# Kernel optimization log

Hardware: AMD Instinct MI355X
Metric: run time of the kernel (lower is better)

## Reference

```python
import jax, jax.numpy as jnp
import numpy as np

N_NODES = 100000


def gcn_conv(x, W, b, src, dst, n):
    # PyG GCNConv: h = x @ W; add self-loops; sym-normalize; scatter-add to dst; + bias
    h = x @ W  # [N, out]
    loops = jnp.arange(n, dtype=src.dtype)
    src2 = jnp.concatenate([src, loops])
    dst2 = jnp.concatenate([dst, loops])
    deg = jax.ops.segment_sum(jnp.ones_like(dst2, dtype=h.dtype), dst2, num_segments=n)
    dinv = jnp.where(deg > 0, jax.lax.rsqrt(deg), 0.0)
    norm = dinv[src2] * dinv[dst2]  # [E+N]
    msg = h[src2] * norm[:, None]   # gather + scale
    out = jax.ops.segment_sum(msg, dst2, num_segments=n)  # scatter-add
    return out + b


def setup_inputs() -> dict:
    key = jax.random.key(0)
    k = jax.random.split(key, 6)
    N, F_IN, H, E = N_NODES, 128, 100, 3200000
    x = jax.random.normal(k[0], (N, F_IN), dtype=jnp.float32)
    edge_index = jax.random.randint(k[1], (2, E), 0, N, dtype=jnp.int64)
    W1 = jax.random.normal(k[2], (F_IN, H), dtype=jnp.float32) / np.sqrt(F_IN).astype(np.float32)
    b1 = jax.random.normal(k[3], (H,), dtype=jnp.float32) * 0.01
    W2 = jax.random.normal(k[4], (H, 1), dtype=jnp.float32) / np.sqrt(H).astype(np.float32)
    b2 = jax.random.normal(k[5], (1,), dtype=jnp.float32) * 0.01
    return {"x": x, "edge_index": edge_index, "W1": W1, "b1": b1, "W2": W2, "b2": b2}


def reference(x, edge_index, W1, b1, W2, b2) -> jnp.ndarray:
    src, dst = edge_index[0], edge_index[1]
    h = gcn_conv(x, W1, b1, src, dst, N_NODES)
    h = jax.nn.relu(h)
    out = gcn_conv(h, W2, b2, src, dst, N_NODES)  # [N, 1]
    return out
```

## Files before the change

kernel.cpp:

```cpp
#include <hip/hip_runtime.h>

#define F_IN 128
#define H1 100
#define G1LD 128
#define CAP 80
#define CH_A 4096
#define NBIN_MAX 256

__device__ __forceinline__ unsigned short f2bf(float f) {
    union { float f; unsigned u; } x;
    x.f = f;
    unsigned u = x.u;
    u += 0x7FFF + ((u >> 16) & 1);
    return (unsigned short)(u >> 16);
}
__device__ __forceinline__ float bflo(unsigned v) {
    union { unsigned u; float f; } x;
    x.u = v << 16;
    return x.f;
}
__device__ __forceinline__ float bfhi(unsigned v) {
    union { unsigned u; float f; } x;
    x.u = v & 0xFFFF0000u;
    return x.f;
}

__global__ __launch_bounds__(256) void k_histA(const int* __restrict__ dst, int* __restrict__ M,
                                               int E, int n, int nbin, int nbA) {
    __shared__ int hist[NBIN_MAX];
    const int tid = threadIdx.x;
    hist[tid] = 0;
    __syncthreads();
    const int base = blockIdx.x * CH_A;
    const int lim = min(CH_A, E - base);
    for (int j = tid; j < lim; j += 256) {
        unsigned d = (unsigned)dst[base + j];
        if (d >= (unsigned)n) d = 0;
        atomicAdd(&hist[d >> 9], 1);
    }
    __syncthreads();
    for (int b = tid; b < nbin; b += 256) M[b * nbA + blockIdx.x] = hist[b];
}

__global__ __launch_bounds__(256) void k_scanRows(const int* __restrict__ M,
                                                  int* __restrict__ Mscan,
                                                  int* __restrict__ T, int nbA) {
    __shared__ int sd[256];
    const int tid = threadIdx.x;
    const int b = blockIdx.x;
    const int base = tid * 4;
    int c[4];
    int s = 0;
    #pragma unroll
    for (int j = 0; j < 4; ++j) {
        int i = base + j;
        c[j] = (i < nbA) ? M[b * nbA + i] : 0;
        s += c[j];
    }
    const int own = s;
    sd[tid] = s;
    __syncthreads();
    for (int off = 1; off < 256; off <<= 1) {
        int t = (tid >= off) ? sd[tid - off] : 0;
        __syncthreads();
        sd[tid] += t;
        __syncthreads();
    }
    int pre = sd[tid] - own;
    #pragma unroll
    for (int j = 0; j < 4; ++j) {
        int i = base + j;
        if (i < nbA) {
            Mscan[b * nbA + i] = pre;
            pre += c[j];
        }
    }
    if (tid == 255) T[b] = sd[255];
}

__global__ __launch_bounds__(256) void k_scanBins(const int* __restrict__ T,
                                                  int* __restrict__ binBase, int nbin) {
    __shared__ int sd[256];
    const int tid = threadIdx.x;
    const int v = (tid < nbin) ? T[tid] : 0;
    sd[tid] = v;
    __syncthreads();
    for (int off = 1; off < 256; off <<= 1) {
        int t = (tid >= off) ? sd[tid - off] : 0;
        __syncthreads();
        sd[tid] += t;
        __syncthreads();
    }
    if (tid < nbin) binBase[tid] = sd[tid] - v;
}

__global__ __launch_bounds__(256) void k_binC(const int* __restrict__ src, const int* __restrict__ dst,
                                              const int* __restrict__ Mscan, const int* __restrict__ binBase,
                                              unsigned* __restrict__ pk, int E, int n, int nbin, int nbA) {
    __shared__ int hist[NBIN_MAX];
    __shared__ int loff[NBIN_MAX];
    const int tid = threadIdx.x;
    hist[tid] = 0;
    for (int b = tid; b < nbin; b += 256) loff[b] = binBase[b] + Mscan[b * nbA + blockIdx.x];
    __syncthreads();
    const int base = blockIdx.x * CH_A;
    const int lim = min(CH_A, E - base);
    for (int j = tid; j < lim; j += 256) {
        unsigned d = (unsigned)dst[base + j];
        unsigned s = (unsigned)src[base + j];
        if (d >= (unsigned)n) d = 0;
        if (s >= (unsigned)n) s = 0;
        const int bin = d >> 9;
        const int r = atomicAdd(&hist[bin], 1);
        pk[loff[bin] + r] = (s << 9) | (d & 511u);
    }
}

__global__ __launch_bounds__(512) void k_binD(const unsigned* __restrict__ pk,
                                              const int* __restrict__ binBase,
                                              int* __restrict__ ebuf, int* __restrict__ counts,
                                              int E, int n, int nbin) {
    __shared__ int fcnt[512];
    const int tid = threadIdx.x;
    fcnt[tid] = 0;
    __syncthreads();
    const int b = blockIdx.x;
    const int bstart = binBase[b];
    const int bend = (b + 1 < nbin) ? binBase[b + 1] : E;
    for (int j = bstart + tid; j < bend; j += 512) {
        const unsigned v = pk[j];
        const int dlow = (int)(v & 511u);
        const int s = (int)(v >> 9);
        const int r = atomicAdd(&fcnt[dlow], 1);
        if (r < CAP) ebuf[((b << 9) + dlow) * CAP + r] = s;
    }
    __syncthreads();
    const int d = (b << 9) + tid;
    if (d < n) {
        const int c = min(fcnt[tid], CAP);
        counts[d] = fcnt[tid];
        const int cp = min((c + 15) & ~15, CAP);
        int* __restrict__ row = ebuf + d * CAP;
        for (int r = c; r < cp; ++r) row[r] = n;
    }
}

__global__ __launch_bounds__(128) void k_gemm1(
    const float* __restrict__ x, const float* __restrict__ W1,
    const int* __restrict__ counts, unsigned short* __restrict__ g, int n) {
    __shared__ float xs[16][F_IN];
    const int f = threadIdx.x;
    const int nb = blockIdx.x * 16;

    {
        const float4* xv = (const float4*)(x + (long)nb * F_IN);
        float4* xsv = (float4*)&xs[0][0];
        #pragma unroll
        for (int k = 0; k < 4; ++k) {
            const int i = f + k * 128;
            const int node = nb + (i >> 5);
            xsv[i] = (node < n) ? xv[i] : make_float4(0.f, 0.f, 0.f, 0.f);
        }
    }
    __syncthreads();

    const bool act = (f < H1);
    float accv[16];
    #pragma unroll
    for (int v = 0; v < 16; ++v) accv[v] = 0.f;

    for (int kc = 0; kc < F_IN; kc += 8) {
        float w[8];
        #pragma unroll
        for (int j = 0; j < 8; ++j) w[j] = act ? W1[(kc + j) * H1 + f] : 0.0f;
        #pragma unroll
        for (int v = 0; v < 16; ++v) {
            const float4 b0 = *(const float4*)&xs[v][kc];
            const float4 b1 = *(const float4*)&xs[v][kc + 4];
            float s = accv[v];
            s = fmaf(b0.x, w[0], s);
            s = fmaf(b0.y, w[1], s);
            s = fmaf(b0.z, w[2], s);
            s = fmaf(b0.w, w[3], s);
            s = fmaf(b1.x, w[4], s);
            s = fmaf(b1.y, w[5], s);
            s = fmaf(b1.z, w[6], s);
            s = fmaf(b1.w, w[7], s);
            accv[v] = s;
        }
    }

    if (act) {
        #pragma unroll
        for (int v = 0; v < 16; ++v) {
            const int node = nb + v;
            if (node < n) {
                const float di = rsqrtf(1.0f + (float)counts[node]);
                g[(node << 7) + f] = f2bf(accv[v] * di);
            } else if (node == n) {
                g[(node << 7) + f] = 0;
            }
        }
    }
}

__global__ __launch_bounds__(256) void k_agg1(
    const unsigned short* __restrict__ g1, const int* __restrict__ counts,
    const int* __restrict__ ebuf,
    const float* __restrict__ b1, const float* __restrict__ W2,
    float* __restrict__ g2, int n) {
    const int lane = threadIdx.x & 63;
    const int node = blockIdx.x * 4 + (threadIdx.x >> 6);
    if (node >= n) return;

    const int c = counts[node];
    const int cnt = (c < CAP) ? c : CAP;
    const int cntp = min((cnt + 15) & ~15, CAP);
    const int4* __restrict__ ebq = (const int4*)(ebuf + node * CAP);
    const unsigned* __restrict__ gp = (const unsigned*)g1;

    const unsigned v0 = gp[(node << 6) + lane];
    float pa0 = bflo(v0), pa1 = 0.f, pa2 = 0.f, pa3 = 0.f;
    float pb0 = bfhi(v0), pb1 = 0.f, pb2 = 0.f, pb3 = 0.f;

    for (int j = 0; j < cntp; j += 16) {
        const int4 e0 = ebq[(j >> 2)];
        const int4 e1 = ebq[(j >> 2) + 1];
        const int4 e2 = ebq[(j >> 2) + 2];
        const int4 e3 = ebq[(j >> 2) + 3];
        const unsigned w0 = gp[(e0.x << 6) + lane];
        const unsigned w1 = gp[(e0.y << 6) + lane];
        const unsigned w2 = gp[(e0.z << 6) + lane];
        const unsigned w3 = gp[(e0.w << 6) + lane];
        const unsigned w4 = gp[(e1.x << 6) + lane];
        const unsigned w5 = gp[(e1.y << 6) + lane];
        const unsigned w6 = gp[(e1.z << 6) + lane];
        const unsigned w7 = gp[(e1.w << 6) + lane];
        const unsigned w8 = gp[(e2.x << 6) + lane];
        const unsigned w9 = gp[(e2.y << 6) + lane];
        const unsigned wa = gp[(e2.z << 6) + lane];
        const unsigned wb = gp[(e2.w << 6) + lane];
        const unsigned wc = gp[(e3.x << 6) + lane];
        const unsigned wd = gp[(e3.y << 6) + lane];
        const unsigned we = gp[(e3.z << 6) + lane];
        const unsigned wf = gp[(e3.w << 6) + lane];
        pa0 += bflo(w0); pb0 += bfhi(w0);
        pa1 += bflo(w1); pb1 += bfhi(w1);
        pa2 += bflo(w2); pb2 += bfhi(w2);
        pa3 += bflo(w3); pb3 += bfhi(w3);
        pa0 += bflo(w4); pb0 += bfhi(w4);
        pa1 += bflo(w5); pb1 += bfhi(w5);
        pa2 += bflo(w6); pb2 += bfhi(w6);
        pa3 += bflo(w7); pb3 += bfhi(w7);
        pa0 += bflo(w8); pb0 += bfhi(w8);
        pa1 += bflo(w9); pb1 += bfhi(w9);
        pa2 += bflo(wa); pb2 += bfhi(wa);
        pa3 += bflo(wb); pb3 += bfhi(wb);
        pa0 += bflo(wc); pb0 += bfhi(wc);
        pa1 += bflo(wd); pb1 += bfhi(wd);
        pa2 += bflo(we); pb2 += bfhi(we);
        pa3 += bflo(wf); pb3 += bfhi(wf);
    }

    const float di = rsqrtf(1.0f + (float)c);
    float sum = 0.f;
    if (lane < H1 / 2) {
        const float sa = (pa0 + pa1) + (pa2 + pa3);
        const float sb = (pb0 + pb1) + (pb2 + pb3);
        const float2 bb = ((const float2*)b1)[lane];
        const float2 ww = ((const float2*)W2)[lane];
        sum = fmaxf(fmaf(di, sa, bb.x), 0.f) * ww.x + fmaxf(fmaf(di, sb, bb.y), 0.f) * ww.y;
    }
    #pragma unroll
    for (int off = 32; off > 0; off >>= 1) sum += __shfl_down(sum, off);
    if (lane == 0) g2[node] = di * sum;
}

__global__ __launch_bounds__(256) void k_agg2(
    const float* __restrict__ g2, const int* __restrict__ counts,
    const int* __restrict__ ebuf, const float* __restrict__ b2,
    float* __restrict__ out, int n) {
    const int lane = threadIdx.x & 63;
    const int node = blockIdx.x * 4 + (threadIdx.x >> 6);
    if (node >= n) return;
    const int c = counts[node];
    const int cnt = (c < CAP) ? c : CAP;
    const int* __restrict__ eb = ebuf + node * CAP;
    float s = 0.f;
    for (int j = lane; j < cnt; j += 64) s += g2[eb[j]];
    #pragma unroll
    for (int off = 32; off > 0; off >>= 1) s += __shfl_down(s, off);
    if (lane == 0) {
        float di = rsqrtf(1.0f + (float)c);
        out[node] = fmaf(di, g2[node] + s, b2[0]);
    }
}

extern "C" void kernel_launch(void* const* d_in, const int* in_sizes, int n_in,
                              void* d_out, int out_size, void* d_ws, size_t ws_size,
                              hipStream_t stream) {
    const float* x  = (const float*)d_in[0];
    const int*   ei = (const int*)d_in[1];
    const float* W1 = (const float*)d_in[2];
    const float* b1 = (const float*)d_in[3];
    const float* W2 = (const float*)d_in[4];
    const float* b2 = (const float*)d_in[5];

    const int n = in_sizes[0] / F_IN;
    const int E = in_sizes[1] / 2;
    const int* src = ei;
    const int* dst = ei + E;

    const int nbin = (n + 511) >> 9;
    const int nbA  = (E + CH_A - 1) / CH_A;
    const int m    = nbin * nbA;

    char* p = (char*)d_ws;
    int* counts = (int*)p;                   p += (size_t)n * 4;
    float* g2   = (float*)p;                 p += (size_t)n * 4;
    p = (char*)(((size_t)p + 255) & ~(size_t)255);
    unsigned short* g1 = (unsigned short*)p; p += (size_t)(n + 1) * G1LD * 2;
    p = (char*)(((size_t)p + 255) & ~(size_t)255);
    int* ebuf   = (int*)p;                   p += (size_t)n * CAP * 4;
    unsigned* pk = (unsigned*)p;             p += (size_t)E * 4;
    int* M      = (int*)p;                   p += (size_t)m * 4;
    int* Mscan  = (int*)p;                   p += (size_t)m * 4;
    int* T      = (int*)p;                   p += 1024;
    int* binBase = (int*)p;                  p += 1024;
    float* out = (float*)d_out;

    k_histA<<<nbA, 256, 0, stream>>>(dst, M, E, n, nbin, nbA);
    k_scanRows<<<nbin, 256, 0, stream>>>(M, Mscan, T, nbA);
    k_scanBins<<<1, 256, 0, stream>>>(T, binBase, nbin);
    k_binC<<<nbA, 256, 0, stream>>>(src, dst, Mscan, binBase, pk, E, n, nbin, nbA);
    k_binD<<<nbin, 512, 0, stream>>>(pk, binBase, ebuf, counts, E, n, nbin);
    k_gemm1<<<(n + 16) / 16, 128, 0, stream>>>(x, W1, counts, g1, n);
    k_agg1<<<(n + 3) / 4, 256, 0, stream>>>(g1, counts, ebuf, b1, W2, g2, n);
    k_agg2<<<(n + 3) / 4, 256, 0, stream>>>(g2, counts, ebuf, b2, out, n);
}
```

Before: 357.5 us.

## Register-tile GEMM1 4x4, pack 4 nodes per wave with 16B gathers in agg1

The first-layer GEMM now uses a 4-node by 4-feature register tile per thread over 20-node blocks, with float4 loads of W1 and vectorized bf16 stores. The first aggregation assigns 16 lanes per node, so each wave handles 4 nodes and each lane gathers a 16-byte uint4 of bf16 features per neighbor. Padding of edge lists in binD is dropped; out-of-range slots are instead masked to a dummy zero row inside agg1. The aim is fewer wasted lanes on 100-wide rows and better load efficiency, at the cost of loops that run to the largest neighbor count among the 4 nodes in a wave.

```diff
diff --git a/kernel.cpp b/kernel.cpp
--- a/kernel.cpp
+++ b/kernel.cpp
@@ -6,6 +6,7 @@
 #define CAP 80
 #define CH_A 4096
 #define NBIN_MAX 256
+#define GN 20
 
 __device__ __forceinline__ unsigned short f2bf(float f) {
     union { float f; unsigned u; } x;
@@ -136,69 +137,78 @@
     }
     __syncthreads();
     const int d = (b << 9) + tid;
-    if (d < n) {
-        const int c = min(fcnt[tid], CAP);
-        counts[d] = fcnt[tid];
-        const int cp = min((c + 15) & ~15, CAP);
-        int* __restrict__ row = ebuf + d * CAP;
-        for (int r = c; r < cp; ++r) row[r] = n;
-    }
+    if (d < n) counts[d] = fcnt[tid];
 }
 
 __global__ __launch_bounds__(128) void k_gemm1(
     const float* __restrict__ x, const float* __restrict__ W1,
     const int* __restrict__ counts, unsigned short* __restrict__ g, int n) {
-    __shared__ float xs[16][F_IN];
-    const int f = threadIdx.x;
-    const int nb = blockIdx.x * 16;
+    __shared__ float xs[GN][132];
+    const int t = threadIdx.x;
+    const int nb = blockIdx.x * GN;
 
     {
-        const float4* xv = (const float4*)(x + (long)nb * F_IN);
-        float4* xsv = (float4*)&xs[0][0];
+        const float4* xv = (const float4*)(x + (size_t)nb * F_IN);
+        for (int i = t; i < GN * 32; i += 128) {
+            const int v = i >> 5, kq = i & 31;
+            const int node = nb + v;
+            const float4 val = (node < n) ? xv[i] : make_float4(0.f, 0.f, 0.f, 0.f);
+            *(float4*)&xs[v][kq * 4] = val;
+        }
+    }
+    __syncthreads();
+
+    const bool act = (t < 125);
+    const int fi = t % 25;
+    const int vg = min(t / 25, 4);
+    const int f0 = fi * 4, v0 = vg * 4;
+
+    float acc[4][4];
+    #pragma unroll
+    for (int i = 0; i < 4; ++i)
         #pragma unroll
-        for (int k = 0; k < 4; ++k) {
-            const int i = f + k * 128;
-            const int node = nb + (i >> 5);
-            xsv[i] = (node < n) ? xv[i] : make_float4(0.f, 0.f, 0.f, 0.f);
-        }
-    }
-    __syncthreads();
-
-    const bool act = (f < H1);
-    float accv[16];
-    #pragma unroll
-    for (int v = 0; v < 16; ++v) accv[v] = 0.f;
-
-    for (int kc = 0; kc < F_IN; kc += 8) {
-        float w[8];
-        #pragma unroll
-        for (int j = 0; j < 8; ++j) w[j] = act ? W1[(kc + j) * H1 + f] : 0.0f;
-        #pragma unroll
-        for (int v = 0; v < 16; ++v) {
-            const float4 b0 = *(const float4*)&xs[v][kc];
-            const float4 b1 = *(const float4*)&xs[v][kc + 4];
-            float s = accv[v];
-            s = fmaf(b0.x, w[0], s);
-            s = fmaf(b0.y, w[1], s);
-            s = fmaf(b0.z, w[2], s);
-            s = fmaf(b0.w, w[3], s);
-            s = fmaf(b1.x, w[4], s);
-            s = fmaf(b1.y, w[5], s);
-            s = fmaf(b1.z, w[6], s);
-            s = fmaf(b1.w, w[7], s);
-            accv[v] = s;
-        }
+        for (int j = 0; j < 4; ++j) acc[i][j] = 0.f;
+
+    const float4* __restrict__ Wf4 = (const float4*)W1;
+    #pragma unroll 4
+    for (int k = 0; k < F_IN; ++k) {
+        const float4 wv = Wf4[k * 25 + fi];
+        const float x0 = xs[v0][k];
+        const float x1 = xs[v0 + 1][k];
+        const float x2 = xs[v0 + 2][k];
+        const float x3 = xs[v0 + 3][k];
+        acc[0][0] = fmaf(x0, wv.x, acc[0][0]);
+        acc[0][1] = fmaf(x0, wv.y, acc[0][1]);
+        acc[0][2] = fmaf(x0, wv.z, acc[0][2]);
+        acc[0][3] = fmaf(x0, wv.w, acc[0][3]);
+        acc[1][0] = fmaf(x1, wv.x, acc[1][0]);
+        acc[1][1] = fmaf(x1, wv.y, acc[1][1]);
+        acc[1][2] = fmaf(x1, wv.z, acc[1][2]);
+        acc[1][3] = fmaf(x1, wv.w, acc[1][3]);
+        acc[2][0] = fmaf(x2, wv.x, acc[2][0]);
+        acc[2][1] = fmaf(x2, wv.y, acc[2][1]);
+        acc[2][2] = fmaf(x2, wv.z, acc[2][2]);
+        acc[2][3] = fmaf(x2, wv.w, acc[2][3]);
+        acc[3][0] = fmaf(x3, wv.x, acc[3][0]);
+        acc[3][1] = fmaf(x3, wv.y, acc[3][1]);
+        acc[3][2] = fmaf(x3, wv.z, acc[3][2]);
+        acc[3][3] = fmaf(x3, wv.w, acc[3][3]);
     }
 
     if (act) {
         #pragma unroll
-        for (int v = 0; v < 16; ++v) {
-            const int node = nb + v;
+        for (int i = 0; i < 4; ++i) {
+            const int node = nb + v0 + i;
             if (node < n) {
                 const float di = rsqrtf(1.0f + (float)counts[node]);
-                g[(node << 7) + f] = f2bf(accv[v] * di);
+                ushort4 o;
+                o.x = f2bf(acc[i][0] * di);
+                o.y = f2bf(acc[i][1] * di);
+                o.z = f2bf(acc[i][2] * di);
+                o.w = f2bf(acc[i][3] * di);
+                *(ushort4*)&g[(node << 7) + f0] = o;
             } else if (node == n) {
-                g[(node << 7) + f] = 0;
+                *(ushort4*)&g[(node << 7) + f0] = make_ushort4(0, 0, 0, 0);
             }
         }
     }
@@ -210,70 +220,64 @@
     const float* __restrict__ b1, const float* __restrict__ W2,
     float* __restrict__ g2, int n) {
     const int lane = threadIdx.x & 63;
-    const int node = blockIdx.x * 4 + (threadIdx.x >> 6);
-    if (node >= n) return;
-
-    const int c = counts[node];
-    const int cnt = (c < CAP) ? c : CAP;
-    const int cntp = min((cnt + 15) & ~15, CAP);
-    const int4* __restrict__ ebq = (const int4*)(ebuf + node * CAP);
-    const unsigned* __restrict__ gp = (const unsigned*)g1;
-
-    const unsigned v0 = gp[(node << 6) + lane];
-    float pa0 = bflo(v0), pa1 = 0.f, pa2 = 0.f, pa3 = 0.f;
-    float pb0 = bfhi(v0), pb1 = 0.f, pb2 = 0.f, pb3 = 0.f;
-
-    for (int j = 0; j < cntp; j += 16) {
-        const int4 e0 = ebq[(j >> 2)];
-        const int4 e1 = ebq[(j >> 2) + 1];
-        const int4 e2 = ebq[(j >> 2) + 2];
-        const int4 e3 = ebq[(j >> 2) + 3];
-        const unsigned w0 = gp[(e0.x << 6) + lane];
-        const unsigned w1 = gp[(e0.y << 6) + lane];
-        const unsigned w2 = gp[(e0.z << 6) + lane];
-        const unsigned w3 = gp[(e0.w << 6) + lane];
-        const unsigned w4 = gp[(e1.x << 6) + lane];
-        const unsigned w5 = gp[(e1.y << 6) + lane];
-        const unsigned w6 = gp[(e1.z << 6) + lane];
-        const unsigned w7 = gp[(e1.w << 6) + lane];
-        const unsigned w8 = gp[(e2.x << 6) + lane];
-        const unsigned w9 = gp[(e2.y << 6) + lane];
-        const unsigned wa = gp[(e2.z << 6) + lane];
-        const unsigned wb = gp[(e2.w << 6) + lane];
-        const unsigned wc = gp[(e3.x << 6) + lane];
-        const unsigned wd = gp[(e3.y << 6) + lane];
-        const unsigned we = gp[(e3.z << 6) + lane];
-        const unsigned wf = gp[(e3.w << 6) + lane];
-        pa0 += bflo(w0); pb0 += bfhi(w0);
-        pa1 += bflo(w1); pb1 += bfhi(w1);
-        pa2 += bflo(w2); pb2 += bfhi(w2);
-        pa3 += bflo(w3); pb3 += bfhi(w3);
-        pa0 += bflo(w4); pb0 += bfhi(w4);
-        pa1 += bflo(w5); pb1 += bfhi(w5);
-        pa2 += bflo(w6); pb2 += bfhi(w6);
-        pa3 += bflo(w7); pb3 += bfhi(w7);
-        pa0 += bflo(w8); pb0 += bfhi(w8);
-        pa1 += bflo(w9); pb1 += bfhi(w9);
-        pa2 += bflo(wa); pb2 += bfhi(wa);
-        pa3 += bflo(wb); pb3 += bfhi(wb);
-        pa0 += bflo(wc); pb0 += bfhi(wc);
-        pa1 += bflo(wd); pb1 += bfhi(wd);
-        pa2 += bflo(we); pb2 += bfhi(we);
-        pa3 += bflo(wf); pb3 += bfhi(wf);
+    const int fl = lane & 15;
+    const int wave = threadIdx.x >> 6;
+    const int node = blockIdx.x * 16 + wave * 4 + (lane >> 4);
+    const int nodec = min(node, n - 1);
+
+    const int c = counts[nodec];
+    const int cnt = min(c, CAP);
+    int cmax = cnt;
+    cmax = max(cmax, __shfl_xor(cmax, 16));
+    cmax = max(cmax, __shfl_xor(cmax, 32));
+
+    const int* __restrict__ eb = ebuf + nodec * CAP;
+    const uint4* __restrict__ gp = (const uint4*)g1;
+
+    uint4 w = gp[(nodec << 4) + fl];
+    float2 a0 = make_float2(bflo(w.x), bfhi(w.x));
+    float2 a1 = make_float2(bflo(w.y), bfhi(w.y));
+    float2 a2 = make_float2(bflo(w.z), bfhi(w.z));
+    float2 a3 = make_float2(bflo(w.w), bfhi(w.w));
+
+    #pragma unroll 2
+    for (int j = 0; j < cmax; ++j) {
+        int e = eb[j];
+        e = (j < cnt) ? e : n;
+        w = gp[(e << 4) + fl];
+        a0.x += bflo(w.x); a0.y += bfhi(w.x);
+        a1.x += bflo(w.y); a1.y += bfhi(w.y);
+        a2.x += bflo(w.z); a2.y += bfhi(w.z);
+        a3.x += bflo(w.w); a3.y += bfhi(w.w);
     }
 
     const float di = rsqrtf(1.0f + (float)c);
     float sum = 0.f;
-    if (lane < H1 / 2) {
-        const float sa = (pa0 + pa1) + (pa2 + pa3);
-        const float sb = (pb0 + pb1) + (pb2 + pb3);
-        const float2 bb = ((const float2*)b1)[lane];
-        const float2 ww = ((const float2*)W2)[lane];
-        sum = fmaxf(fmaf(di, sa, bb.x), 0.f) * ww.x + fmaxf(fmaf(di, sb, bb.y), 0.f) * ww.y;
-    }
-    #pragma unroll
-    for (int off = 32; off > 0; off >>= 1) sum += __shfl_down(sum, off);
-    if (lane == 0) g2[node] = di * sum;
+    const int fbase = fl * 8;
+    if (fbase < H1) {
+        const float4 ba = ((const float4*)b1)[fl * 2];
+        const float4 wa = ((const float4*)W2)[fl * 2];
+        float s;
+        s  = fmaxf(fmaf(di, a0.x, ba.x), 0.f) * wa.x;
+        s += fmaxf(fmaf(di, a0.y, ba.y), 0.f) * wa.y;
+        s += fmaxf(fmaf(di, a1.x, ba.z), 0.f) * wa.z;
+        s += fmaxf(fmaf(di, a1.y, ba.w), 0.f) * wa.w;
+        sum = s;
+        if (fbase + 4 < H1) {
+            const float4 bb = ((const float4*)b1)[fl * 2 + 1];
+            const float4 wb = ((const float4*)W2)[fl * 2 + 1];
+            s  = fmaxf(fmaf(di, a2.x, bb.x), 0.f) * wb.x;
+            s += fmaxf(fmaf(di, a2.y, bb.y), 0.f) * wb.y;
+            s += fmaxf(fmaf(di, a3.x, bb.z), 0.f) * wb.z;
+            s += fmaxf(fmaf(di, a3.y, bb.w), 0.f) * wb.w;
+            sum += s;
+        }
+    }
+    sum += __shfl_xor(sum, 1);
+    sum += __shfl_xor(sum, 2);
+    sum += __shfl_xor(sum, 4);
+    sum += __shfl_xor(sum, 8);
+    if (fl == 0 && node < n) g2[node] = di * sum;
 }
 
 __global__ __launch_bounds__(256) void k_agg2(
@@ -334,7 +338,7 @@
     k_scanBins<<<1, 256, 0, stream>>>(T, binBase, nbin);
     k_binC<<<nbA, 256, 0, stream>>>(src, dst, Mscan, binBase, pk, E, n, nbin, nbA);
     k_binD<<<nbin, 512, 0, stream>>>(pk, binBase, ebuf, counts, E, n, nbin);
-    k_gemm1<<<(n + 16) / 16, 128, 0, stream>>>(x, W1, counts, g1, n);
-    k_agg1<<<(n + 3) / 4, 256, 0, stream>>>(g1, counts, ebuf, b1, W2, g2, n);
+    k_gemm1<<<(n + GN) / GN, 128, 0, stream>>>(x, W1, counts, g1, n);
+    k_agg1<<<(n + 15) / 16, 256, 0, stream>>>(g1, counts, ebuf, b1, W2, g2, n);
     k_agg2<<<(n + 3) / 4, 256, 0, stream>>>(g2, counts, ebuf, b2, out, n);
 }
```

Result: no change. 350.6 us (-1.9%).

## Stage binning scatter in LDS and retile GEMM1 to 4x4 register blocks

Applied to the files above, without the earlier changes.

The binning scatter kernel now uses larger chunks of 15360 edges per 512-thread block. It counting-sorts each chunk into shared memory first, then writes runs to global memory that are contiguous per bin, which makes the previously scattered global stores coalesced. The first GEMM is retiled so each thread computes a 4-node by 4-feature block using float4 loads of W1 and padded shared rows, with vectorized bf16 stores. This adds a serial prefix scan by a single thread, binary searches per element, large LDS usage that lowers occupancy, and a second read of dst.

```diff
diff --git a/kernel.cpp b/kernel.cpp
--- a/kernel.cpp
+++ b/kernel.cpp
@@ -4,8 +4,9 @@
 #define H1 100
 #define G1LD 128
 #define CAP 80
-#define CH_A 4096
+#define CH_S 15360
 #define NBIN_MAX 256
+#define GN 20
 
 __device__ __forceinline__ unsigned short f2bf(float f) {
     union { float f; unsigned u; } x;
@@ -25,21 +26,21 @@
     return x.f;
 }
 
-__global__ __launch_bounds__(256) void k_histA(const int* __restrict__ dst, int* __restrict__ M,
+__global__ __launch_bounds__(512) void k_histA(const int* __restrict__ dst, int* __restrict__ M,
                                                int E, int n, int nbin, int nbA) {
     __shared__ int hist[NBIN_MAX];
     const int tid = threadIdx.x;
-    hist[tid] = 0;
-    __syncthreads();
-    const int base = blockIdx.x * CH_A;
-    const int lim = min(CH_A, E - base);
-    for (int j = tid; j < lim; j += 256) {
+    for (int b = tid; b < nbin; b += 512) hist[b] = 0;
+    __syncthreads();
+    const int base = blockIdx.x * CH_S;
+    const int lim = min(CH_S, E - base);
+    for (int j = tid; j < lim; j += 512) {
         unsigned d = (unsigned)dst[base + j];
         if (d >= (unsigned)n) d = 0;
         atomicAdd(&hist[d >> 9], 1);
     }
     __syncthreads();
-    for (int b = tid; b < nbin; b += 256) M[b * nbA + blockIdx.x] = hist[b];
+    for (int b = tid; b < nbin; b += 512) M[b * nbA + blockIdx.x] = hist[b];
 }
 
 __global__ __launch_bounds__(256) void k_scanRows(const int* __restrict__ M,
@@ -94,25 +95,55 @@
     if (tid < nbin) binBase[tid] = sd[tid] - v;
 }
 
-__global__ __launch_bounds__(256) void k_binC(const int* __restrict__ src, const int* __restrict__ dst,
-                                              const int* __restrict__ Mscan, const int* __restrict__ binBase,
-                                              unsigned* __restrict__ pk, int E, int n, int nbin, int nbA) {
+__global__ __launch_bounds__(512) void k_sortC(const int* __restrict__ src, const int* __restrict__ dst,
+                                               const int* __restrict__ Mscan, const int* __restrict__ binBase,
+                                               unsigned* __restrict__ pk, int E, int n, int nbin, int nbA) {
+    __shared__ unsigned staged[CH_S];
     __shared__ int hist[NBIN_MAX];
+    __shared__ int offs[NBIN_MAX + 1];
     __shared__ int loff[NBIN_MAX];
     const int tid = threadIdx.x;
-    hist[tid] = 0;
-    for (int b = tid; b < nbin; b += 256) loff[b] = binBase[b] + Mscan[b * nbA + blockIdx.x];
-    __syncthreads();
-    const int base = blockIdx.x * CH_A;
-    const int lim = min(CH_A, E - base);
-    for (int j = tid; j < lim; j += 256) {
+    for (int b = tid; b < nbin; b += 512) {
+        hist[b] = 0;
+        loff[b] = binBase[b] + Mscan[b * nbA + blockIdx.x];
+    }
+    __syncthreads();
+    const int base = blockIdx.x * CH_S;
+    const int lim = min(CH_S, E - base);
+
+    for (int j = tid; j < lim; j += 512) {
+        unsigned d = (unsigned)dst[base + j];
+        if (d >= (unsigned)n) d = 0;
+        atomicAdd(&hist[d >> 9], 1);
+    }
+    __syncthreads();
+    if (tid == 0) {
+        int a = 0;
+        for (int b = 0; b < nbin; ++b) { offs[b] = a; a += hist[b]; }
+        offs[nbin] = a;
+    }
+    __syncthreads();
+    for (int b = tid; b < nbin; b += 512) hist[b] = 0;
+    __syncthreads();
+
+    for (int j = tid; j < lim; j += 512) {
         unsigned d = (unsigned)dst[base + j];
         unsigned s = (unsigned)src[base + j];
         if (d >= (unsigned)n) d = 0;
         if (s >= (unsigned)n) s = 0;
         const int bin = d >> 9;
         const int r = atomicAdd(&hist[bin], 1);
-        pk[loff[bin] + r] = (s << 9) | (d & 511u);
+        staged[offs[bin] + r] = (s << 9) | (d & 511u);
+    }
+    __syncthreads();
+
+    for (int i = tid; i < lim; i += 512) {
+        int lo = 0, hi = nbin;
+        while (hi - lo > 1) {
+            const int mid = (lo + hi) >> 1;
+            if (offs[mid] <= i) lo = mid; else hi = mid;
+        }
+        pk[loff[lo] + (i - offs[lo])] = staged[i];
     }
 }
 
@@ -148,57 +179,72 @@
 __global__ __launch_bounds__(128) void k_gemm1(
     const float* __restrict__ x, const float* __restrict__ W1,
     const int* __restrict__ counts, unsigned short* __restrict__ g, int n) {
-    __shared__ float xs[16][F_IN];
-    const int f = threadIdx.x;
-    const int nb = blockIdx.x * 16;
+    __shared__ float xs[GN][132];
+    const int t = threadIdx.x;
+    const int nb = blockIdx.x * GN;
 
     {
-        const float4* xv = (const float4*)(x + (long)nb * F_IN);
-        float4* xsv = (float4*)&xs[0][0];
+        const float4* xv = (const float4*)(x + (size_t)nb * F_IN);
+        for (int i = t; i < GN * 32; i += 128) {
+            const int v = i >> 5, kq = i & 31;
+            const int node = nb + v;
+            const float4 val = (node < n) ? xv[i] : make_float4(0.f, 0.f, 0.f, 0.f);
+            *(float4*)&xs[v][kq * 4] = val;
+        }
+    }
+    __syncthreads();
+
+    const bool act = (t < 125);
+    const int fi = t % 25;
+    const int vg = min(t / 25, 4);
+    const int f0 = fi * 4, v0 = vg * 4;
+
+    float acc[4][4];
+    #pragma unroll
+    for (int i = 0; i < 4; ++i)
         #pragma unroll
-        for (int k = 0; k < 4; ++k) {
-            const int i = f + k * 128;
-            const int node = nb + (i >> 5);
-            xsv[i] = (node < n) ? xv[i] : make_float4(0.f, 0.f, 0.f, 0.f);
-        }
-    }
-    __syncthreads();
-
-    const bool act = (f < H1);
-    float accv[16];
-    #pragma unroll
-    for (int v = 0; v < 16; ++v) accv[v] = 0.f;
-
-    for (int kc = 0; kc < F_IN; kc += 8) {
-        float w[8];
-        #pragma unroll
-        for (int j = 0; j < 8; ++j) w[j] = act ? W1[(kc + j) * H1 + f] : 0.0f;
-        #pragma unroll
-        for (int v = 0; v < 16; ++v) {
-            const float4 b0 = *(const float4*)&xs[v][kc];
-            const float4 b1 = *(const float4*)&xs[v][kc + 4];
-            float s = accv[v];
-            s = fmaf(b0.x, w[0], s);
-            s = fmaf(b0.y, w[1], s);
-            s = fmaf(b0.z, w[2], s);
-            s = fmaf(b0.w, w[3], s);
-            s = fmaf(b1.x, w[4], s);
-            s = fmaf(b1.y, w[5], s);
-            s = fmaf(b1.z, w[6], s);
-            s = fmaf(b1.w, w[7], s);
-            accv[v] = s;
-        }
+        for (int j = 0; j < 4; ++j) acc[i][j] = 0.f;
+
+    const float4* __restrict__ Wf4 = (const float4*)W1;
+    #pragma unroll 4
+    for (int k = 0; k < F_IN; ++k) {
+        const float4 wv = Wf4[k * 25 + fi];
+        const float x0 = xs[v0][k];
+        const float x1 = xs[v0 + 1][k];
+        const float x2 = xs[v0 + 2][k];
+        const float x3 = xs[v0 + 3][k];
+        acc[0][0] = fmaf(x0, wv.x, acc[0][0]);
+        acc[0][1] = fmaf(x0, wv.y, acc[0][1]);
+        acc[0][2] = fmaf(x0, wv.z, acc[0][2]);
+        acc[0][3] = fmaf(x0, wv.w, acc[0][3]);
+        acc[1][0] = fmaf(x1, wv.x, acc[1][0]);
+        acc[1][1] = fmaf(x1, wv.y, acc[1][1]);
+        acc[1][2] = fmaf(x1, wv.z, acc[1][2]);
+        acc[1][3] = fmaf(x1, wv.w, acc[1][3]);
+        acc[2][0] = fmaf(x2, wv.x, acc[2][0]);
+        acc[2][1] = fmaf(x2, wv.y, acc[2][1]);
+        acc[2][2] = fmaf(x2, wv.z, acc[2][2]);
+        acc[2][3] = fmaf(x2, wv.w, acc[2][3]);
+        acc[3][0] = fmaf(x3, wv.x, acc[3][0]);
+        acc[3][1] = fmaf(x3, wv.y, acc[3][1]);
+        acc[3][2] = fmaf(x3, wv.z, acc[3][2]);
+        acc[3][3] = fmaf(x3, wv.w, acc[3][3]);
     }
 
     if (act) {
         #pragma unroll
-        for (int v = 0; v < 16; ++v) {
-            const int node = nb + v;
+        for (int i = 0; i < 4; ++i) {
+            const int node = nb + v0 + i;
             if (node < n) {
                 const float di = rsqrtf(1.0f + (float)counts[node]);
-                g[(node << 7) + f] = f2bf(accv[v] * di);
+                ushort4 o;
+                o.x = f2bf(acc[i][0] * di);
+                o.y = f2bf(acc[i][1] * di);
+                o.z = f2bf(acc[i][2] * di);
+                o.w = f2bf(acc[i][3] * di);
+                *(ushort4*)&g[(node << 7) + f0] = o;
             } else if (node == n) {
-                g[(node << 7) + f] = 0;
+                *(ushort4*)&g[(node << 7) + f0] = make_ushort4(0, 0, 0, 0);
             }
         }
     }
@@ -264,11 +310,12 @@
 
     const float di = rsqrtf(1.0f + (float)c);
     float sum = 0.f;
-    if (lane < H1 / 2) {
-        const float sa = (pa0 + pa1) + (pa2 + pa3);
-        const float sb = (pb0 + pb1) + (pb2 + pb3);
+    const int fbase = lane * 2;
+    if (fbase < H1) {
         const float2 bb = ((const float2*)b1)[lane];
         const float2 ww = ((const float2*)W2)[lane];
+        const float sa = ((pa0 + pa1) + (pa2 + pa3));
+        const float sb = ((pb0 + pb1) + (pb2 + pb3));
         sum = fmaxf(fmaf(di, sa, bb.x), 0.f) * ww.x + fmaxf(fmaf(di, sb, bb.y), 0.f) * ww.y;
     }
     #pragma unroll
@@ -312,8 +359,8 @@
     const int* dst = ei + E;
 
     const int nbin = (n + 511) >> 9;
-    const int nbA  = (E + CH_A - 1) / CH_A;
-    const int m    = nbin * nbA;
+    const int nbS  = (E + CH_S - 1) / CH_S;
+    const int m    = nbin * nbS;
 
     char* p = (char*)d_ws;
     int* counts = (int*)p;                   p += (size_t)n * 4;
@@ -329,12 +376,12 @@
     int* binBase = (int*)p;                  p += 1024;
     float* out = (float*)d_out;
 
-    k_histA<<<nbA, 256, 0, stream>>>(dst, M, E, n, nbin, nbA);
-    k_scanRows<<<nbin, 256, 0, stream>>>(M, Mscan, T, nbA);
+    k_histA<<<nbS, 512, 0, stream>>>(dst, M, E, n, nbin, nbS);
+    k_scanRows<<<nbin, 256, 0, stream>>>(M, Mscan, T, nbS);
     k_scanBins<<<1, 256, 0, stream>>>(T, binBase, nbin);
-    k_binC<<<nbA, 256, 0, stream>>>(src, dst, Mscan, binBase, pk, E, n, nbin, nbA);
+    k_sortC<<<nbS, 512, 0, stream>>>(src, dst, Mscan, binBase, pk, E, n, nbin, nbS);
     k_binD<<<nbin, 512, 0, stream>>>(pk, binBase, ebuf, counts, E, n, nbin);
-    k_gemm1<<<(n + 16) / 16, 128, 0, stream>>>(x, W1, counts, g1, n);
+    k_gemm1<<<(n + GN) / GN, 128, 0, stream>>>(x, W1, counts, g1, n);
     k_agg1<<<(n + 3) / 4, 256, 0, stream>>>(g1, counts, ebuf, b1, W2, g2, n);
     k_agg2<<<(n + 3) / 4, 256, 0, stream>>>(g2, counts, ebuf, b2, out, n);
 }
```

New measurement: 351.4 us. About the same (-1.7%).
